# Kernel optimization log

Hardware: AMD Instinct MI355X
Metric: run time of the kernel (lower is better)

## Reference

```python
import jax, jax.numpy as jnp
import numpy as np

CHANNELS = 256
LAYERS = 4
IN_FEAT = 118
N_NODES = 20000
N_EDGES = 320000


def setup_inputs() -> dict:
    key = jax.random.key(0)
    ks = jax.random.split(key, 4 + 4 * LAYERS)
    x = jax.random.normal(ks[0], (N_NODES, IN_FEAT), dtype=jnp.float32)
    edge_index = jax.random.randint(ks[1], (2, N_EDGES), 0, N_NODES, dtype=jnp.int64)
    s = 1.0 / np.sqrt(CHANNELS)
    W_embed = jax.random.normal(ks[2], (IN_FEAT, CHANNELS), dtype=jnp.float32) / np.sqrt(IN_FEAT)
    b_embed = jnp.zeros((CHANNELS,), dtype=jnp.float32)
    W1 = jax.random.normal(ks[3], (LAYERS, CHANNELS, CHANNELS), dtype=jnp.float32) * s
    b1 = jnp.zeros((LAYERS, CHANNELS), dtype=jnp.float32)
    W2 = jax.random.normal(ks[4], (LAYERS, CHANNELS, CHANNELS), dtype=jnp.float32) * s
    b2 = jnp.zeros((LAYERS, CHANNELS), dtype=jnp.float32)
    return {"x": x, "edge_index": edge_index, "W_embed": W_embed, "b_embed": b_embed,
            "W1": W1, "b1": b1, "W2": W2, "b2": b2}


def reference(x, edge_index, W_embed, b_embed, W1, b1, W2, b2):
    n = x.shape[0]
    src, dst = edge_index[0], edge_index[1]
    # in-degree for mean aggregation (constant across layers)
    cnt = jax.ops.segment_sum(jnp.ones(src.shape[0], dtype=x.dtype), dst, num_segments=n)
    inv_cnt = (1.0 / jnp.maximum(cnt, 1.0))[:, None]
    h = x @ W_embed + b_embed  # [N, C]
    for l in range(W1.shape[0]):
        # message: gather source features, dense + exact GELU (dropout off in eval)
        msg = jax.nn.gelu(h[src] @ W1[l] + b1[l], approximate=False)  # [E, C]
        # mean-scatter aggregate over destination nodes
        agg = jax.ops.segment_sum(msg, dst, num_segments=n) * inv_cnt  # [N, C]
        # update: dense + GELU
        h = jax.nn.gelu(agg @ W2[l] + b2[l], approximate=False)
    return jnp.mean(h, axis=1)  # [N]
```

## Files before the change

kernel.cpp:

```cpp
#include <hip/hip_runtime.h>
#include <math.h>

#define CH 256

typedef _Float16 half8 __attribute__((ext_vector_type(8)));
typedef _Float16 half4 __attribute__((ext_vector_type(4)));
typedef float f32x4 __attribute__((ext_vector_type(4)));

__device__ __forceinline__ float gelu_exact(float v) {
    return 0.5f * v * (1.0f + erff(v * 0.70710678118654752f));
}

__global__ void wsplit_kernel(const float* __restrict__ W1, const float* __restrict__ W2,
                              _Float16* __restrict__ WThi, _Float16* __restrict__ WTlo) {
    int idx = blockIdx.x * blockDim.x + threadIdx.x;
    int n   = idx & 255;
    int kg  = (idx >> 8) & 31;
    int mat = idx >> 13;
    const float* W = (mat < 4) ? (W1 + (size_t)mat * 65536)
                               : (W2 + (size_t)(mat - 4) * 65536);
    _Float16 hi[8], lo[8];
#pragma unroll
    for (int j = 0; j < 8; j++) {
        float v = W[(size_t)(kg * 8 + j) * CH + n];
        _Float16 h = (_Float16)v;
        hi[j] = h;
        lo[j] = (_Float16)(v - (float)h);
    }
    size_t off = (size_t)mat * 65536 + (size_t)n * 256 + kg * 8;
    *(half8*)(WThi + off) = *(half8*)&hi[0];
    *(half8*)(WTlo + off) = *(half8*)&lo[0];
}

__global__ void wesplit_kernel(const float* __restrict__ We,
                               _Float16* __restrict__ WeTh, _Float16* __restrict__ WeTl) {
    int idx = blockIdx.x * blockDim.x + threadIdx.x;
    if (idx >= 4096) return;
    int n  = idx >> 4;
    int k8 = (idx & 15) * 8;
    _Float16 hi[8], lo[8];
#pragma unroll
    for (int j = 0; j < 8; j++) {
        int k = k8 + j;
        float v = (k < 118) ? We[(size_t)k * CH + n] : 0.f;
        _Float16 h = (_Float16)v;
        hi[j] = h;
        lo[j] = (_Float16)(v - (float)h);
    }
    size_t off = (size_t)n * 128 + k8;
    *(half8*)(WeTh + off) = *(half8*)&hi[0];
    *(half8*)(WeTl + off) = *(half8*)&lo[0];
}

__global__ void xsplit_kernel(const float* __restrict__ x,
                              _Float16* __restrict__ xh, _Float16* __restrict__ xl, int N) {
    int idx = blockIdx.x * blockDim.x + threadIdx.x;
    int n  = idx >> 4;
    int c8 = (idx & 15) * 8;
    if (n >= N) return;
    _Float16 hi[8], lo[8];
#pragma unroll
    for (int j = 0; j < 8; j++) {
        int c = c8 + j;
        float v = (c < 118) ? x[(size_t)n * 118 + c] : 0.f;
        _Float16 h = (_Float16)v;
        hi[j] = h;
        lo[j] = (_Float16)(v - (float)h);
    }
    size_t off = (size_t)n * 128 + c8;
    *(half8*)(xh + off) = *(half8*)&hi[0];
    *(half8*)(xl + off) = *(half8*)&lo[0];
}

template<int KT, bool DOGELU>
__global__ __launch_bounds__(256, 4) void mgemm_kernel(
    const _Float16* __restrict__ Ah_g, const _Float16* __restrict__ Al_g,
    const _Float16* __restrict__ Bh_g, const _Float16* __restrict__ Bl_g,
    const float* __restrict__ bias,
    _Float16* __restrict__ Oh, _Float16* __restrict__ Ol,
    int M, int MC)
{
    const int KLEN = KT * 32;
    __shared__ _Float16 Ah[128][40], Al[128][40], Bh[64][40], Bl[64][40];

    int b    = blockIdx.x;
    int xcd  = b & 7;
    int slot = b >> 3;
    int mt   = xcd * MC + (slot >> 2);
    int nt   = slot & 3;
    if (mt * 128 >= M) return;
    int m0 = mt * 128;
    int n0 = nt * 64;

    int tid  = threadIdx.x;
    int lane = tid & 63;
    int wave = tid >> 6;
    int wr = wave >> 1;
    int wc = wave & 1;

    f32x4 acc[4][2];
#pragma unroll
    for (int i = 0; i < 4; i++)
#pragma unroll
        for (int j = 0; j < 2; j++) acc[i][j] = (f32x4){0.f, 0.f, 0.f, 0.f};

    const int s_row = tid >> 1;
    const int s_ch  = (tid & 1) * 16;
    const size_t s_arow = (size_t)min(m0 + s_row, M - 1);
    const int bcol = (tid & 127) >> 1;
    const int bch  = (tid & 1) * 16;

    for (int kt = 0; kt < KT; kt++) {
        int k0 = kt * 32;
        {
            const _Float16* sh_ = Ah_g + s_arow * KLEN + k0 + s_ch;
            const _Float16* sl_ = Al_g + s_arow * KLEN + k0 + s_ch;
            half8 h0 = ((const half8*)sh_)[0];
            half8 h1 = ((const half8*)sh_)[1];
            half8 l0 = ((const half8*)sl_)[0];
            half8 l1 = ((const half8*)sl_)[1];
            *(half8*)&Ah[s_row][s_ch]     = h0;
            *(half8*)&Ah[s_row][s_ch + 8] = h1;
            *(half8*)&Al[s_row][s_ch]     = l0;
            *(half8*)&Al[s_row][s_ch + 8] = l1;
        }
        {
            const _Float16* bs = ((tid < 128) ? Bh_g : Bl_g)
                                 + (size_t)(n0 + bcol) * KLEN + k0 + bch;
            half8 u0 = ((const half8*)bs)[0];
            half8 u1 = ((const half8*)bs)[1];
            _Float16 (*dst)[40] = (tid < 128) ? Bh : Bl;
            *(half8*)&dst[bcol][bch]     = u0;
            *(half8*)&dst[bcol][bch + 8] = u1;
        }
        __syncthreads();

        {
            int frow = lane & 15;
            int fk   = (lane >> 4) * 8;
            half8 ah[4], al[4], bh[2], bl[2];
#pragma unroll
            for (int rf = 0; rf < 4; rf++) {
                int r = wr * 64 + rf * 16 + frow;
                ah[rf] = *(const half8*)&Ah[r][fk];
                al[rf] = *(const half8*)&Al[r][fk];
            }
#pragma unroll
            for (int cf = 0; cf < 2; cf++) {
                int c = wc * 32 + cf * 16 + frow;
                bh[cf] = *(const half8*)&Bh[c][fk];
                bl[cf] = *(const half8*)&Bl[c][fk];
            }
#pragma unroll
            for (int rf = 0; rf < 4; rf++)
#pragma unroll
                for (int cf = 0; cf < 2; cf++) {
                    acc[rf][cf] = __builtin_amdgcn_mfma_f32_16x16x32_f16(ah[rf], bh[cf], acc[rf][cf], 0, 0, 0);
                    acc[rf][cf] = __builtin_amdgcn_mfma_f32_16x16x32_f16(ah[rf], bl[cf], acc[rf][cf], 0, 0, 0);
                    acc[rf][cf] = __builtin_amdgcn_mfma_f32_16x16x32_f16(al[rf], bh[cf], acc[rf][cf], 0, 0, 0);
                }
        }
        __syncthreads();
    }

    int ccol = lane & 15;
    int crow = (lane >> 4) * 4;
#pragma unroll
    for (int cf = 0; cf < 2; cf++) {
        int gcol = n0 + wc * 32 + cf * 16 + ccol;
        float bb = bias[gcol];
#pragma unroll
        for (int rf = 0; rf < 4; rf++) {
#pragma unroll
            for (int q = 0; q < 4; q++) {
                int grow = m0 + wr * 64 + rf * 16 + crow + q;
                if (grow < M) {
                    float v = acc[rf][cf][q] + bb;
                    float g = DOGELU ? gelu_exact(v) : v;
                    _Float16 hi = (_Float16)g;
                    Oh[(size_t)grow * CH + gcol] = hi;
                    Ol[(size_t)grow * CH + gcol] = (_Float16)(g - (float)hi);
                }
            }
        }
    }
}

__global__ void zero_int_kernel(int* p, int n) {
    int i = blockIdx.x * blockDim.x + threadIdx.x;
    if (i < n) p[i] = 0;
}

__global__ void degree_kernel(const int* __restrict__ ei, int E, int* deg) {
    int e = blockIdx.x * blockDim.x + threadIdx.x;
    if (e < E) atomicAdd(&deg[ei[E + e]], 1);
}

__global__ void scan_part_kernel(const int* __restrict__ deg, int* bsum, int N) {
    int t = threadIdx.x;
    int base = blockIdx.x * 1024 + t * 4;
    int4 v = {0, 0, 0, 0};
    if (base + 3 < N) v = *(const int4*)(deg + base);
    else {
        if (base + 0 < N) v.x = deg[base + 0];
        if (base + 1 < N) v.y = deg[base + 1];
        if (base + 2 < N) v.z = deg[base + 2];
        if (base + 3 < N) v.w = deg[base + 3];
    }
    __shared__ int sh[256];
    sh[t] = v.x + v.y + v.z + v.w;
    __syncthreads();
    for (int off = 128; off; off >>= 1) {
        if (t < off) sh[t] += sh[t + off];
        __syncthreads();
    }
    if (t == 0) bsum[blockIdx.x] = sh[0];
}

__global__ void scan_top_kernel(const int* __restrict__ bsum, int* boff, int B) {
    __shared__ int sh[256];
    int t = threadIdx.x;
    int own = (t < B) ? bsum[t] : 0;
    sh[t] = own;
    __syncthreads();
    for (int off = 1; off < 256; off <<= 1) {
        int v = (t >= off) ? sh[t - off] : 0;
        __syncthreads();
        sh[t] += v;
        __syncthreads();
    }
    if (t < B) boff[t] = sh[t] - own;
}

__global__ void scan_final_kernel(const int* __restrict__ deg, const int* __restrict__ boff,
                                  int* row_ptr, int* fill_pos, float* inv, int N, int E) {
    int t = threadIdx.x;
    int base = blockIdx.x * 1024 + t * 4;
    int4 v = {0, 0, 0, 0};
    if (base + 3 < N) v = *(const int4*)(deg + base);
    else {
        if (base + 0 < N) v.x = deg[base + 0];
        if (base + 1 < N) v.y = deg[base + 1];
        if (base + 2 < N) v.z = deg[base + 2];
        if (base + 3 < N) v.w = deg[base + 3];
    }
    int own = v.x + v.y + v.z + v.w;
    __shared__ int sh[256];
    sh[t] = own;
    __syncthreads();
    for (int off = 1; off < 256; off <<= 1) {
        int s = (t >= off) ? sh[t - off] : 0;
        __syncthreads();
        sh[t] += s;
        __syncthreads();
    }
    int run = boff[blockIdx.x] + (sh[t] - own);
    int4 rp;
    rp.x = run;
    rp.y = run + v.x;
    rp.z = rp.y + v.y;
    rp.w = rp.z + v.z;
    if (base + 3 < N) {
        *(int4*)(row_ptr + base) = rp;
        *(int4*)(fill_pos + base) = rp;
        float4 iv;
        iv.x = 1.0f / fmaxf((float)v.x, 1.0f);
        iv.y = 1.0f / fmaxf((float)v.y, 1.0f);
        iv.z = 1.0f / fmaxf((float)v.z, 1.0f);
        iv.w = 1.0f / fmaxf((float)v.w, 1.0f);
        *(float4*)(inv + base) = iv;
    } else {
        int rr[4] = {rp.x, rp.y, rp.z, rp.w};
        int dd[4] = {v.x, v.y, v.z, v.w};
        for (int q = 0; q < 4; q++) {
            if (base + q < N) {
                row_ptr[base + q] = rr[q];
                fill_pos[base + q] = rr[q];
                inv[base + q] = 1.0f / fmaxf((float)dd[q], 1.0f);
            }
        }
    }
    if (blockIdx.x == 0 && t == 0) row_ptr[N] = E;
}

__global__ void fill_kernel(const int* __restrict__ ei, int E, int* fill_pos, int* colv) {
    int e = blockIdx.x * blockDim.x + threadIdx.x;
    if (e < E) {
        int p = atomicAdd(&fill_pos[ei[E + e]], 1);
        colv[p] = ei[e];
    }
}

__global__ void agg_kernel(const _Float16* __restrict__ th, const _Float16* __restrict__ tl,
                           const int* __restrict__ row_ptr, const int* __restrict__ colv,
                           const float* __restrict__ inv,
                           _Float16* __restrict__ aggh, _Float16* __restrict__ aggl, int N) {
    int n = blockIdx.x * 4 + (threadIdx.x >> 6);
    if (n >= N) return;
    int lane = threadIdx.x & 63;
    int s = row_ptr[n], e = row_ptr[n + 1];
    size_t loff = (size_t)lane * 4;

    f32x4 a0 = {0.f, 0.f, 0.f, 0.f}, a1 = a0, a2 = a0, a3 = a0;
    int j = s;
    for (; j + 4 <= e; j += 4) {
        int c0 = colv[j], c1 = colv[j + 1], c2 = colv[j + 2], c3 = colv[j + 3];
        half4 h0 = *(const half4*)(th + (size_t)c0 * CH + loff);
        half4 l0 = *(const half4*)(tl + (size_t)c0 * CH + loff);
        half4 h1 = *(const half4*)(th + (size_t)c1 * CH + loff);
        half4 l1 = *(const half4*)(tl + (size_t)c1 * CH + loff);
        half4 h2 = *(const half4*)(th + (size_t)c2 * CH + loff);
        half4 l2 = *(const half4*)(tl + (size_t)c2 * CH + loff);
        half4 h3 = *(const half4*)(th + (size_t)c3 * CH + loff);
        half4 l3 = *(const half4*)(tl + (size_t)c3 * CH + loff);
#pragma unroll
        for (int q = 0; q < 4; q++) {
            a0[q] += (float)h0[q] + (float)l0[q];
            a1[q] += (float)h1[q] + (float)l1[q];
            a2[q] += (float)h2[q] + (float)l2[q];
            a3[q] += (float)h3[q] + (float)l3[q];
        }
    }
    for (; j < e; j++) {
        int c = colv[j];
        half4 h = *(const half4*)(th + (size_t)c * CH + loff);
        half4 l = *(const half4*)(tl + (size_t)c * CH + loff);
#pragma unroll
        for (int q = 0; q < 4; q++) a0[q] += (float)h[q] + (float)l[q];
    }
    f32x4 tot = (a0 + a1) + (a2 + a3);
    float sc = inv[n];
    _Float16 oh[4], ol[4];
#pragma unroll
    for (int q = 0; q < 4; q++) {
        float v = tot[q] * sc;
        _Float16 hi = (_Float16)v;
        oh[q] = hi;
        ol[q] = (_Float16)(v - (float)hi);
    }
    *(half4*)(aggh + (size_t)n * CH + loff) = *(half4*)&oh[0];
    *(half4*)(aggl + (size_t)n * CH + loff) = *(half4*)&ol[0];
}

__global__ void mean_kernel(const _Float16* __restrict__ hh, const _Float16* __restrict__ hl,
                            float* __restrict__ out, int N) {
    int n = blockIdx.x * 4 + (threadIdx.x >> 6);
    if (n >= N) return;
    int lane = threadIdx.x & 63;
    half4 vh = *(const half4*)(hh + (size_t)n * CH + lane * 4);
    half4 vl = *(const half4*)(hl + (size_t)n * CH + lane * 4);
    float s = 0.f;
#pragma unroll
    for (int q = 0; q < 4; q++) s += (float)vh[q] + (float)vl[q];
#pragma unroll
    for (int off = 32; off; off >>= 1) s += __shfl_down(s, off, 64);
    if (lane == 0) out[n] = s * (1.0f / 256.0f);
}

extern "C" void kernel_launch(void* const* d_in, const int* in_sizes, int n_in,
                              void* d_out, int out_size, void* d_ws, size_t ws_size,
                              hipStream_t stream) {
    const float* x       = (const float*)d_in[0];
    const int*   ei      = (const int*)d_in[1];
    const float* W_embed = (const float*)d_in[2];
    const float* b_embed = (const float*)d_in[3];
    const float* W1      = (const float*)d_in[4];
    const float* b1      = (const float*)d_in[5];
    const float* W2      = (const float*)d_in[6];
    const float* b2      = (const float*)d_in[7];
    float* out = (float*)d_out;

    int N = in_sizes[0] / 118;
    int E = in_sizes[1] / 2;
    int SB = (N + 1023) / 1024;
    size_t NC = (size_t)N * CH;

    _Float16* hh   = (_Float16*)d_ws;
    _Float16* hl   = hh + NC;
    _Float16* th   = hl + NC;
    _Float16* tl   = th + NC;
    _Float16* ah   = tl + NC;
    _Float16* al   = ah + NC;
    _Float16* WThi = al + NC;
    _Float16* WTlo = WThi + 8 * 65536;
    _Float16* WeTh = WTlo + 8 * 65536;
    _Float16* WeTl = WeTh + 256 * 128;
    float*    inv      = (float*)(WeTl + 256 * 128);
    int*      deg      = (int*)(inv + N);
    int*      row_ptr  = deg + N;
    int*      fill_pos = row_ptr + (N + 1);
    int*      colv     = fill_pos + N;
    int*      bsum     = colv + E;
    int*      boff     = bsum + 256;

    _Float16* xh = th;
    _Float16* xl = th + (size_t)N * 128;

    zero_int_kernel<<<(N + 255) / 256, 256, 0, stream>>>(deg, N);
    degree_kernel<<<(E + 255) / 256, 256, 0, stream>>>(ei, E, deg);
    scan_part_kernel<<<SB, 256, 0, stream>>>(deg, bsum, N);
    scan_top_kernel<<<1, 256, 0, stream>>>(bsum, boff, SB);
    scan_final_kernel<<<SB, 256, 0, stream>>>(deg, boff, row_ptr, fill_pos, inv, N, E);
    fill_kernel<<<(E + 255) / 256, 256, 0, stream>>>(ei, E, fill_pos, colv);
    wsplit_kernel<<<256, 256, 0, stream>>>(W1, W2, WThi, WTlo);
    wesplit_kernel<<<16, 256, 0, stream>>>(W_embed, WeTh, WeTl);
    xsplit_kernel<<<(N * 16 + 255) / 256, 256, 0, stream>>>(x, xh, xl, N);

    int mtiles = (N + 127) / 128;
    int MC = (mtiles + 7) / 8;
    int mgrid = 8 * MC * 4;

    mgemm_kernel<4, false><<<mgrid, 256, 0, stream>>>(xh, xl, WeTh, WeTl, b_embed,
                                                      hh, hl, N, MC);
    for (int l = 0; l < 4; l++) {
        mgemm_kernel<8, true><<<mgrid, 256, 0, stream>>>(hh, hl,
                                                         WThi + (size_t)l * 65536,
                                                         WTlo + (size_t)l * 65536,
                                                         b1 + (size_t)l * CH, th, tl, N, MC);
        agg_kernel<<<(N + 3) / 4, 256, 0, stream>>>(th, tl, row_ptr, colv, inv, ah, al, N);
        mgemm_kernel<8, true><<<mgrid, 256, 0, stream>>>(ah, al,
                                                         WThi + (size_t)(4 + l) * 65536,
                                                         WTlo + (size_t)(4 + l) * 65536,
                                                         b2 + (size_t)l * CH, hh, hl, N, MC);
    }
    mean_kernel<<<(N + 3) / 4, 256, 0, stream>>>(hh, hl, out, N);
}
```

Before: 443.4 us.

## Store GEMM operands in K-tiled layout and stage epilogue through LDS

Changes the A and B operand layouts (weights, x, aggregated features, hidden state) to K-blocked tiles of 32 halves so each GEMM k-step loads one contiguous 8 KB panel with a single 16-byte load per thread. The epilogue now packs hi/lo halves into LDS and writes coalesced 32-bit pairs, in either the tiled or the row-major layout depending on the consumer. Rows are padded to a multiple of 128 so the bounds checks can go. The cost is extra LDS round-trips and syncs in the epilogue, plus larger workspace buffers.

```diff
diff --git a/kernel.cpp b/kernel.cpp
--- a/kernel.cpp
+++ b/kernel.cpp
@@ -1,5 +1,6 @@
 #include <hip/hip_runtime.h>
 #include <math.h>
+#include <stdint.h>
 
 #define CH 256
 
@@ -27,7 +28,7 @@
         hi[j] = h;
         lo[j] = (_Float16)(v - (float)h);
     }
-    size_t off = (size_t)mat * 65536 + (size_t)n * 256 + kg * 8;
+    size_t off = (size_t)mat * 65536 + ((size_t)(kg >> 2) * 256 + n) * 32 + (kg & 3) * 8;
     *(half8*)(WThi + off) = *(half8*)&hi[0];
     *(half8*)(WTlo + off) = *(half8*)&lo[0];
 }
@@ -47,13 +48,14 @@
         hi[j] = h;
         lo[j] = (_Float16)(v - (float)h);
     }
-    size_t off = (size_t)n * 128 + k8;
+    size_t off = ((size_t)(k8 >> 5) * 256 + n) * 32 + (k8 & 31);
     *(half8*)(WeTh + off) = *(half8*)&hi[0];
     *(half8*)(WeTl + off) = *(half8*)&lo[0];
 }
 
 __global__ void xsplit_kernel(const float* __restrict__ x,
-                              _Float16* __restrict__ xh, _Float16* __restrict__ xl, int N) {
+                              _Float16* __restrict__ xh, _Float16* __restrict__ xl,
+                              int N, int Mpad) {
     int idx = blockIdx.x * blockDim.x + threadIdx.x;
     int n  = idx >> 4;
     int c8 = (idx & 15) * 8;
@@ -67,28 +69,32 @@
         hi[j] = h;
         lo[j] = (_Float16)(v - (float)h);
     }
-    size_t off = (size_t)n * 128 + c8;
+    size_t off = ((size_t)(c8 >> 5) * Mpad + n) * 32 + (c8 & 31);
     *(half8*)(xh + off) = *(half8*)&hi[0];
     *(half8*)(xl + off) = *(half8*)&lo[0];
 }
 
-template<int KT, bool DOGELU>
+template<int KT, bool DOGELU, bool TILED>
 __global__ __launch_bounds__(256, 4) void mgemm_kernel(
     const _Float16* __restrict__ Ah_g, const _Float16* __restrict__ Al_g,
     const _Float16* __restrict__ Bh_g, const _Float16* __restrict__ Bl_g,
     const float* __restrict__ bias,
     _Float16* __restrict__ Oh, _Float16* __restrict__ Ol,
-    int M, int MC)
+    int Mpad, int MC)
 {
-    const int KLEN = KT * 32;
-    __shared__ _Float16 Ah[128][40], Al[128][40], Bh[64][40], Bl[64][40];
+    __shared__ __align__(16) char smem[30720];
+    _Float16 (*Ah)[40] = (_Float16(*)[40])smem;
+    _Float16 (*Al)[40] = (_Float16(*)[40])(smem + 10240);
+    _Float16 (*Bh)[40] = (_Float16(*)[40])(smem + 20480);
+    _Float16 (*Bl)[40] = (_Float16(*)[40])(smem + 25600);
+    uint32_t (*Obuf)[68] = (uint32_t(*)[68])smem;
 
     int b    = blockIdx.x;
     int xcd  = b & 7;
     int slot = b >> 3;
     int mt   = xcd * MC + (slot >> 2);
     int nt   = slot & 3;
-    if (mt * 128 >= M) return;
+    if (mt * 128 >= Mpad) return;
     int m0 = mt * 128;
     int n0 = nt * 64;
 
@@ -104,35 +110,27 @@
 #pragma unroll
         for (int j = 0; j < 2; j++) acc[i][j] = (f32x4){0.f, 0.f, 0.f, 0.f};
 
-    const int s_row = tid >> 1;
-    const int s_ch  = (tid & 1) * 16;
-    const size_t s_arow = (size_t)min(m0 + s_row, M - 1);
-    const int bcol = (tid & 127) >> 1;
-    const int bch  = (tid & 1) * 16;
+    const int Lb    = tid * 8;
+    const int arow0 = Lb >> 5;
+    const int ak    = Lb & 31;
 
     for (int kt = 0; kt < KT; kt++) {
-        int k0 = kt * 32;
-        {
-            const _Float16* sh_ = Ah_g + s_arow * KLEN + k0 + s_ch;
-            const _Float16* sl_ = Al_g + s_arow * KLEN + k0 + s_ch;
-            half8 h0 = ((const half8*)sh_)[0];
-            half8 h1 = ((const half8*)sh_)[1];
-            half8 l0 = ((const half8*)sl_)[0];
-            half8 l1 = ((const half8*)sl_)[1];
-            *(half8*)&Ah[s_row][s_ch]     = h0;
-            *(half8*)&Ah[s_row][s_ch + 8] = h1;
-            *(half8*)&Al[s_row][s_ch]     = l0;
-            *(half8*)&Al[s_row][s_ch + 8] = l1;
-        }
-        {
-            const _Float16* bs = ((tid < 128) ? Bh_g : Bl_g)
-                                 + (size_t)(n0 + bcol) * KLEN + k0 + bch;
-            half8 u0 = ((const half8*)bs)[0];
-            half8 u1 = ((const half8*)bs)[1];
-            _Float16 (*dst)[40] = (tid < 128) ? Bh : Bl;
-            *(half8*)&dst[bcol][bch]     = u0;
-            *(half8*)&dst[bcol][bch + 8] = u1;
-        }
+        const _Float16* pah = Ah_g + ((size_t)kt * Mpad + m0) * 32;
+        const _Float16* pal = Al_g + ((size_t)kt * Mpad + m0) * 32;
+        const _Float16* pbh = Bh_g + ((size_t)kt * 256 + n0) * 32;
+        const _Float16* pbl = Bl_g + ((size_t)kt * 256 + n0) * 32;
+        half8 a0 = *(const half8*)(pah + Lb);
+        half8 a1 = *(const half8*)(pah + 2048 + Lb);
+        half8 a2 = *(const half8*)(pal + Lb);
+        half8 a3 = *(const half8*)(pal + 2048 + Lb);
+        half8 b0 = *(const half8*)(pbh + Lb);
+        half8 b1 = *(const half8*)(pbl + Lb);
+        *(half8*)&Ah[arow0][ak]      = a0;
+        *(half8*)&Ah[64 + arow0][ak] = a1;
+        *(half8*)&Al[arow0][ak]      = a2;
+        *(half8*)&Al[64 + arow0][ak] = a3;
+        *(half8*)&Bh[arow0][ak]      = b0;
+        *(half8*)&Bl[arow0][ak]      = b1;
         __syncthreads();
 
         {
@@ -165,24 +163,45 @@
 
     int ccol = lane & 15;
     int crow = (lane >> 4) * 4;
-#pragma unroll
-    for (int cf = 0; cf < 2; cf++) {
-        int gcol = n0 + wc * 32 + cf * 16 + ccol;
-        float bb = bias[gcol];
-#pragma unroll
-        for (int rf = 0; rf < 4; rf++) {
-#pragma unroll
-            for (int q = 0; q < 4; q++) {
-                int grow = m0 + wr * 64 + rf * 16 + crow + q;
-                if (grow < M) {
-                    float v = acc[rf][cf][q] + bb;
-                    float g = DOGELU ? gelu_exact(v) : v;
-                    _Float16 hi = (_Float16)g;
-                    Oh[(size_t)grow * CH + gcol] = hi;
-                    Ol[(size_t)grow * CH + gcol] = (_Float16)(g - (float)hi);
-                }
-            }
+    float bb[2];
+    bb[0] = bias[n0 + wc * 32 + ccol];
+    bb[1] = bias[n0 + wc * 32 + 16 + ccol];
+#pragma unroll
+    for (int half = 0; half < 2; half++) {
+        if (wr == half) {
+#pragma unroll
+            for (int cf = 0; cf < 2; cf++)
+#pragma unroll
+                for (int rf = 0; rf < 4; rf++)
+#pragma unroll
+                    for (int q = 0; q < 4; q++) {
+                        float v = acc[rf][cf][q] + bb[cf];
+                        float g = DOGELU ? gelu_exact(v) : v;
+                        _Float16 hi = (_Float16)g;
+                        _Float16 lo = (_Float16)(g - (float)hi);
+                        uint32_t u = (uint32_t)__builtin_bit_cast(uint16_t, hi)
+                                   | ((uint32_t)__builtin_bit_cast(uint16_t, lo) << 16);
+                        Obuf[rf * 16 + crow + q][wc * 32 + cf * 16 + ccol] = u;
+                    }
         }
+        __syncthreads();
+#pragma unroll
+        for (int i = 0; i < 8; i++) {
+            int idx = i * 512 + tid * 2;
+            int row = idx >> 6;
+            int c   = idx & 63;
+            uint32_t u0 = Obuf[row][c];
+            uint32_t u1 = Obuf[row][c + 1];
+            uint32_t hi2 = (u0 & 0xffffu) | (u1 << 16);
+            uint32_t lo2 = (u0 >> 16) | (u1 & 0xffff0000u);
+            int grow = m0 + half * 64 + row;
+            int gcol = n0 + c;
+            size_t off = TILED ? ((size_t)(gcol >> 5) * Mpad + grow) * 32 + (gcol & 31)
+                               : (size_t)grow * CH + gcol;
+            *(uint32_t*)(Oh + off) = hi2;
+            *(uint32_t*)(Ol + off) = lo2;
+        }
+        __syncthreads();
     }
 }
 
@@ -294,7 +313,8 @@
 __global__ void agg_kernel(const _Float16* __restrict__ th, const _Float16* __restrict__ tl,
                            const int* __restrict__ row_ptr, const int* __restrict__ colv,
                            const float* __restrict__ inv,
-                           _Float16* __restrict__ aggh, _Float16* __restrict__ aggl, int N) {
+                           _Float16* __restrict__ aggh, _Float16* __restrict__ aggl,
+                           int N, int Mpad) {
     int n = blockIdx.x * 4 + (threadIdx.x >> 6);
     if (n >= N) return;
     int lane = threadIdx.x & 63;
@@ -338,22 +358,24 @@
         oh[q] = hi;
         ol[q] = (_Float16)(v - (float)hi);
     }
-    *(half4*)(aggh + (size_t)n * CH + loff) = *(half4*)&oh[0];
-    *(half4*)(aggl + (size_t)n * CH + loff) = *(half4*)&ol[0];
+    size_t ooff = ((size_t)(lane >> 3) * Mpad + n) * 32 + ((lane * 4) & 31);
+    *(half4*)(aggh + ooff) = *(half4*)&oh[0];
+    *(half4*)(aggl + ooff) = *(half4*)&ol[0];
 }
 
 __global__ void mean_kernel(const _Float16* __restrict__ hh, const _Float16* __restrict__ hl,
-                            float* __restrict__ out, int N) {
+                            float* __restrict__ out, int N, int Mpad) {
     int n = blockIdx.x * 4 + (threadIdx.x >> 6);
     if (n >= N) return;
     int lane = threadIdx.x & 63;
-    half4 vh = *(const half4*)(hh + (size_t)n * CH + lane * 4);
-    half4 vl = *(const half4*)(hl + (size_t)n * CH + lane * 4);
+    size_t off = ((size_t)(lane >> 3) * Mpad + n) * 32 + ((lane * 4) & 31);
+    half4 vh = *(const half4*)(hh + off);
+    half4 vl = *(const half4*)(hl + off);
     float s = 0.f;
 #pragma unroll
     for (int q = 0; q < 4; q++) s += (float)vh[q] + (float)vl[q];
 #pragma unroll
-    for (int off = 32; off; off >>= 1) s += __shfl_down(s, off, 64);
+    for (int off2 = 32; off2; off2 >>= 1) s += __shfl_down(s, off2, 64);
     if (lane == 0) out[n] = s * (1.0f / 256.0f);
 }
 
@@ -373,7 +395,8 @@
     int N = in_sizes[0] / 118;
     int E = in_sizes[1] / 2;
     int SB = (N + 1023) / 1024;
-    size_t NC = (size_t)N * CH;
+    int Mpad = ((N + 127) / 128) * 128;
+    size_t NC = (size_t)Mpad * CH;
 
     _Float16* hh   = (_Float16*)d_ws;
     _Float16* hl   = hh + NC;
@@ -384,8 +407,8 @@
     _Float16* WThi = al + NC;
     _Float16* WTlo = WThi + 8 * 65536;
     _Float16* WeTh = WTlo + 8 * 65536;
-    _Float16* WeTl = WeTh + 256 * 128;
-    float*    inv      = (float*)(WeTl + 256 * 128);
+    _Float16* WeTl = WeTh + 32768;
+    float*    inv      = (float*)(WeTl + 32768);
     int*      deg      = (int*)(inv + N);
     int*      row_ptr  = deg + N;
     int*      fill_pos = row_ptr + (N + 1);
@@ -394,7 +417,7 @@
     int*      boff     = bsum + 256;
 
     _Float16* xh = th;
-    _Float16* xl = th + (size_t)N * 128;
+    _Float16* xl = th + (size_t)Mpad * 128;
 
     zero_int_kernel<<<(N + 255) / 256, 256, 0, stream>>>(deg, N);
     degree_kernel<<<(E + 255) / 256, 256, 0, stream>>>(ei, E, deg);
@@ -404,24 +427,27 @@
     fill_kernel<<<(E + 255) / 256, 256, 0, stream>>>(ei, E, fill_pos, colv);
     wsplit_kernel<<<256, 256, 0, stream>>>(W1, W2, WThi, WTlo);
     wesplit_kernel<<<16, 256, 0, stream>>>(W_embed, WeTh, WeTl);
-    xsplit_kernel<<<(N * 16 + 255) / 256, 256, 0, stream>>>(x, xh, xl, N);
-
-    int mtiles = (N + 127) / 128;
+    xsplit_kernel<<<(N * 16 + 255) / 256, 256, 0, stream>>>(x, xh, xl, N, Mpad);
+
+    int mtiles = Mpad / 128;
     int MC = (mtiles + 7) / 8;
     int mgrid = 8 * MC * 4;
 
-    mgemm_kernel<4, false><<<mgrid, 256, 0, stream>>>(xh, xl, WeTh, WeTl, b_embed,
-                                                      hh, hl, N, MC);
+    mgemm_kernel<4, false, true><<<mgrid, 256, 0, stream>>>(xh, xl, WeTh, WeTl, b_embed,
+                                                            hh, hl, Mpad, MC);
     for (int l = 0; l < 4; l++) {
-        mgemm_kernel<8, true><<<mgrid, 256, 0, stream>>>(hh, hl,
-                                                         WThi + (size_t)l * 65536,
-                                                         WTlo + (size_t)l * 65536,
-                                                         b1 + (size_t)l * CH, th, tl, N, MC);
-        agg_kernel<<<(N + 3) / 4, 256, 0, stream>>>(th, tl, row_ptr, colv, inv, ah, al, N);
-        mgemm_kernel<8, true><<<mgrid, 256, 0, stream>>>(ah, al,
-                                                         WThi + (size_t)(4 + l) * 65536,
-                                                         WTlo + (size_t)(4 + l) * 65536,
-                                                         b2 + (size_t)l * CH, hh, hl, N, MC);
-    }
-    mean_kernel<<<(N + 3) / 4, 256, 0, stream>>>(hh, hl, out, N);
-}
+        mgemm_kernel<8, true, false><<<mgrid, 256, 0, stream>>>(hh, hl,
+                                                                WThi + (size_t)l * 65536,
+                                                                WTlo + (size_t)l * 65536,
+                                                                b1 + (size_t)l * CH,
+                                                                th, tl, Mpad, MC);
+        agg_kernel<<<(N + 3) / 4, 256, 0, stream>>>(th, tl, row_ptr, colv, inv,
+                                                    ah, al, N, Mpad);
+        mgemm_kernel<8, true, true><<<mgrid, 256, 0, stream>>>(ah, al,
+                                                               WThi + (size_t)(4 + l) * 65536,
+                                                               WTlo + (size_t)(4 + l) * 65536,
+                                                               b2 + (size_t)l * CH,
+                                                               hh, hl, Mpad, MC);
+    }
+    mean_kernel<<<(N + 3) / 4, 256, 0, stream>>>(hh, hl, out, N, Mpad);
+}
```

New measurement: 428.2 us. 1.04x faster.
